# Kernel tuning notes

Hardware: AMD Instinct MI355X
Metric: run time of the kernel (lower is better)

The kernel has to match this reference:

```python
import jax, jax.numpy as jnp
import numpy as np

N_NODES = 50000
N_EDGES = 800000


def setup_inputs() -> dict:
    key = jax.random.key(0)
    ks = jax.random.split(key, 8)
    x = jax.random.normal(ks[0], (N_NODES, 256), dtype=jnp.float32)
    edge_index = jax.random.randint(ks[1], (2, N_EDGES), 0, N_NODES, dtype=jnp.int64)
    edge_weight = jax.random.uniform(ks[2], (N_EDGES,), dtype=jnp.float32)
    # Glorot-style weights for the 3 GCNConv layers: 256->128->64->32
    def glorot(k, fan_in, fan_out):
        s = jnp.sqrt(6.0 / (fan_in + fan_out))
        return jax.random.uniform(k, (fan_in, fan_out), dtype=jnp.float32, minval=-s, maxval=s)
    return {
        "x": x,
        "edge_index": edge_index,
        "edge_weight": edge_weight,
        "W1": glorot(ks[3], 256, 128), "b1": jnp.zeros((128,), jnp.float32),
        "W2": glorot(ks[4], 128, 64),  "b2": jnp.zeros((64,), jnp.float32),
        "W3": glorot(ks[5], 64, 32),   "b3": jnp.zeros((32,), jnp.float32),
    }


def _gcn_forward(x, row, col, ew, params):
    """Stacked GCNConv+ReLU (PyG semantics: add self loops, symmetric norm)."""
    n = x.shape[0]
    loop = jnp.arange(n, dtype=row.dtype)
    row_f = jnp.concatenate([row, loop])            # [E+N] sources
    col_f = jnp.concatenate([col, loop])            # [E+N] targets
    ew_f = jnp.concatenate([ew, jnp.ones((n,), ew.dtype)])
    deg = jax.ops.segment_sum(ew_f, col_f, num_segments=n)
    dinv = jnp.where(deg > 0, jax.lax.rsqrt(deg), 0.0)
    norm = dinv[row_f] * ew_f * dinv[col_f]         # [E+N]
    for W, b in params:
        h = x @ W                                   # [N, d_out] linear first (PyG order)
        msg = h[row_f] * norm[:, None]              # [E+N, d_out] gather + scale
        agg = jax.ops.segment_sum(msg, col_f, num_segments=n)  # scatter-add
        x = jax.nn.relu(agg + b)                    # fused bias + ReLU
    return x


def reference(x, edge_index, edge_weight, W1, b1, W2, b2, W3, b3):
    row, col = edge_index[0], edge_index[1]
    params = [(W1, b1), (W2, b2), (W3, b3)]
    return _gcn_forward(x, row, col, edge_weight, params)
```

## Files before the change

kernel.cpp:

```cpp
#include <hip/hip_runtime.h>
#include <hip/hip_fp16.h>


#define D0 256
#define D1 128
#define D2 64
#define D3 32

#define FIX_SCALE 16777216.0f
#define FIX_INV   (1.0f / 16777216.0f)

typedef _Float16 half8 __attribute__((ext_vector_type(8)));
typedef float floatx4 __attribute__((ext_vector_type(4)));

template <typename SRC>
__device__ __forceinline__ half8 loadA(const SRC* __restrict__ p) {
    if constexpr (sizeof(SRC) == 4) {
        float4 f0 = *(const float4*)p;
        float4 f1 = *(const float4*)(p + 4);
        half8 v;
        v[0] = (_Float16)f0.x; v[1] = (_Float16)f0.y;
        v[2] = (_Float16)f0.z; v[3] = (_Float16)f0.w;
        v[4] = (_Float16)f1.x; v[5] = (_Float16)f1.y;
        v[6] = (_Float16)f1.z; v[7] = (_Float16)f1.w;
        return v;
    } else {
        return *(const half8*)p;
    }
}

template <int K, int BN, typename SRC>
__device__ __forceinline__ void gemm_work(const SRC* __restrict__ X,
                                          const float* __restrict__ W,
                                          _Float16* __restrict__ H, int N,
                                          int w, int totalWaves) {
    constexpr int NC = K / 32;
    constexpr int CG = BN / 32;
    const int lane = threadIdx.x & 63;
    const int quad = lane >> 4;
    const int m = lane & 15;
    const int cg = w & (CG - 1);
    const int nslab = N >> 4;
    const int stride = totalWaves / CG;
    int slab = w / CG;
    if (slab >= nslab) return;
    const int n0 = cg * 32;

    half8 b0[NC], b1[NC];
#pragma unroll
    for (int c = 0; c < NC; ++c) {
#pragma unroll
        for (int j = 0; j < 8; ++j) {
            int k = c * 32 + quad * 8 + j;
            b0[c][j] = (_Float16)W[(size_t)k * BN + n0 + m];
            b1[c][j] = (_Float16)W[(size_t)k * BN + n0 + 16 + m];
        }
    }

    half8 a[NC];
#pragma unroll
    for (int c = 0; c < NC; ++c)
        a[c] = loadA(&X[(size_t)(slab * 16 + m) * K + c * 32 + quad * 8]);

    while (true) {
        const int next = slab + stride;
        half8 an[NC];
        if (next < nslab) {
#pragma unroll
            for (int c = 0; c < NC; ++c)
                an[c] = loadA(&X[(size_t)(next * 16 + m) * K + c * 32 + quad * 8]);
        }

        floatx4 acc0 = (floatx4){0.f, 0.f, 0.f, 0.f};
        floatx4 acc1 = (floatx4){0.f, 0.f, 0.f, 0.f};
#pragma unroll
        for (int c = 0; c < NC; ++c) {
            acc0 = __builtin_amdgcn_mfma_f32_16x16x32_f16(a[c], b0[c], acc0, 0, 0, 0);
            acc1 = __builtin_amdgcn_mfma_f32_16x16x32_f16(a[c], b1[c], acc1, 0, 0, 0);
        }

        const int r0 = slab * 16 + quad * 4;
#pragma unroll
        for (int r = 0; r < 4; ++r) {
            H[(size_t)(r0 + r) * BN + n0 + m]      = (_Float16)acc0[r];
            H[(size_t)(r0 + r) * BN + n0 + 16 + m] = (_Float16)acc1[r];
        }

        if (next >= nslab) break;
        slab = next;
#pragma unroll
        for (int c = 0; c < NC; ++c) a[c] = an[c];
    }
}

__global__ __launch_bounds__(256) void hist_gemm1_kernel(
        const float* __restrict__ x, const float* __restrict__ W1,
        _Float16* __restrict__ h1, int N,
        const int* __restrict__ ei, const float* __restrict__ ew,
        unsigned long long* __restrict__ pk, int* __restrict__ rank, int E,
        int gB) {
    const int b = blockIdx.x;
    if (b < gB) {
        gemm_work<D0, D1, float>(x, W1, h1, N, b * 4 + (threadIdx.x >> 6), gB * 4);
    } else {
        int e = (b - gB) * 256 + threadIdx.x;
        if (e < E) {
            int c = ei[E + e];
            unsigned int wfix = (unsigned int)(ew[e] * FIX_SCALE + 0.5f);
            unsigned long long old =
                atomicAdd(&pk[c], (1ULL << 32) | (unsigned long long)wfix);
            rank[e] = (int)(old >> 32);
        }
    }
}

template <int K, int BN, typename SRC>
__global__ __launch_bounds__(256) void mfma_gemm(const SRC* __restrict__ X,
                                                 const float* __restrict__ W,
                                                 _Float16* __restrict__ H, int N) {
    gemm_work<K, BN, SRC>(X, W, H, N, blockIdx.x * 4 + (threadIdx.x >> 6), gridDim.x * 4);
}

__global__ __launch_bounds__(256) void scan_reduce(const unsigned long long* __restrict__ pk,
                                                   float* __restrict__ dinv,
                                                   int* __restrict__ cnt,
                                                   int* __restrict__ blockSum, int N) {
    __shared__ int s[256];
    const int t = threadIdx.x;
    const int i = blockIdx.x * 256 + t;
    int v = 0;
    if (i < N) {
        unsigned long long p = pk[i];
        float d = (float)(unsigned int)(p & 0xffffffffULL) * FIX_INV + 1.0f;
        dinv[i] = rsqrtf(d);
        v = (int)(p >> 32);
        cnt[i] = v;
    }
    s[t] = v;
    __syncthreads();
#pragma unroll
    for (int off = 128; off > 0; off >>= 1) {
        if (t < off) s[t] += s[t + off];
        __syncthreads();
    }
    if (t == 0) blockSum[blockIdx.x] = s[0];
}

__global__ __launch_bounds__(256) void scan_apply(const int* __restrict__ cnt,
                                                  const int* __restrict__ blockSum,
                                                  int* __restrict__ row_ptr, int N, int B) {
    __shared__ int bs[256];
    __shared__ int s[256];
    const int t = threadIdx.x;
    bs[t] = (t < B) ? blockSum[t] : 0;
    __syncthreads();
#pragma unroll
    for (int off = 1; off < 256; off <<= 1) {
        int u = (t >= off) ? bs[t - off] : 0;
        __syncthreads();
        bs[t] += u;
        __syncthreads();
    }
    const int myOff = (blockIdx.x > 0) ? bs[blockIdx.x - 1] : 0;
    const int i = blockIdx.x * 256 + t;
    const int v = (i < N) ? cnt[i] : 0;
    s[t] = v;
    __syncthreads();
#pragma unroll
    for (int off = 1; off < 256; off <<= 1) {
        int u = (t >= off) ? s[t - off] : 0;
        __syncthreads();
        s[t] += u;
        __syncthreads();
    }
    if (i < N) row_ptr[i] = s[t] - v + myOff;
    if (blockIdx.x == 0 && t == 0) row_ptr[N] = bs[B - 1];
}

__global__ void fill_kernel(const int* __restrict__ ei, const float* __restrict__ ew,
                            const float* __restrict__ dinv,
                            const int* __restrict__ row_ptr, const int* __restrict__ rank,
                            int2* __restrict__ pairs, int E) {
    int e = blockIdx.x * blockDim.x + threadIdx.x;
    if (e < E) {
        int r = ei[e];
        int c = ei[E + e];
        float w = dinv[r] * ew[e] * dinv[c];
        pairs[row_ptr[c] + rank[e]] = make_int2(r, __float_as_int(w));
    }
}

template <int D, typename OUT>
__global__ __launch_bounds__(256) void agg_kernel(const _Float16* __restrict__ H,
                                                  const int* __restrict__ row_ptr,
                                                  const int2* __restrict__ pairs,
                                                  const float* __restrict__ dinv,
                                                  const float* __restrict__ bias,
                                                  OUT* __restrict__ out, int N) {
    constexpr int TPN = D / 8;
    constexpr int NPB = 256 / TPN;
    const int tid = threadIdx.x;
    const int g = tid / TPN;
    const int lane = tid % TPN;
    const int node = blockIdx.x * NPB + g;
    if (node >= N) return;

    const int beg = row_ptr[node];
    const int end = row_ptr[node + 1];
    float acc[8];
#pragma unroll
    for (int j = 0; j < 8; ++j) acc[j] = 0.0f;

    if (end > beg) {
        const int last = end - 1;
        int2 p0 = pairs[beg];
        int2 p1 = pairs[min(beg + 1, last)];
        int2 p2 = pairs[min(beg + 2, last)];
        half8 u0 = *(const half8*)&H[(size_t)p0.x * D + lane * 8];
        half8 u1 = *(const half8*)&H[(size_t)p1.x * D + lane * 8];
        for (int k = beg; k < end; ++k) {
            int2 p3 = pairs[min(k + 3, last)];
            half8 u2 = *(const half8*)&H[(size_t)p2.x * D + lane * 8];
            float w = __int_as_float(p0.y);
#pragma unroll
            for (int j = 0; j < 8; ++j) acc[j] = fmaf(w, (float)u0[j], acc[j]);
            p0 = p1; p1 = p2; p2 = p3;
            u0 = u1; u1 = u2;
        }
    }
    float di = dinv[node];
    float d2 = di * di;
    {
        half8 u = *(const half8*)&H[(size_t)node * D + lane * 8];
#pragma unroll
        for (int j = 0; j < 8; ++j) acc[j] = fmaf(d2, (float)u[j], acc[j]);
    }
    float b[8];
    *(float4*)&b[0] = *(const float4*)&bias[lane * 8];
    *(float4*)&b[4] = *(const float4*)&bias[lane * 8 + 4];
#pragma unroll
    for (int j = 0; j < 8; ++j) acc[j] = fmaxf(acc[j] + b[j], 0.f);

    if constexpr (sizeof(OUT) == 2) {
        half8 o;
#pragma unroll
        for (int j = 0; j < 8; ++j) o[j] = (_Float16)acc[j];
        *(half8*)&out[(size_t)node * D + lane * 8] = o;
    } else {
        float* dst = (float*)&out[(size_t)node * D + lane * 8];
        *(float4*)&dst[0] = make_float4(acc[0], acc[1], acc[2], acc[3]);
        *(float4*)&dst[4] = make_float4(acc[4], acc[5], acc[6], acc[7]);
    }
}

extern "C" void kernel_launch(void* const* d_in, const int* in_sizes, int n_in,
                              void* d_out, int out_size, void* d_ws, size_t ws_size,
                              hipStream_t stream) {
    const float* x   = (const float*)d_in[0];
    const int* ei    = (const int*)d_in[1];
    const float* ew  = (const float*)d_in[2];
    const float* W1  = (const float*)d_in[3];
    const float* b1  = (const float*)d_in[4];
    const float* W2  = (const float*)d_in[5];
    const float* b2  = (const float*)d_in[6];
    const float* W3  = (const float*)d_in[7];
    const float* b3  = (const float*)d_in[8];
    float* out = (float*)d_out;

    const int N = in_sizes[0] / D0;
    const int E = in_sizes[2];
    (void)n_in; (void)out_size; (void)ws_size;

    char* ws = (char*)d_ws;
    size_t off = 0;
    auto carve = [&](size_t bytes) -> void* {
        void* p = (void*)(ws + off);
        off += (bytes + 255) & ~(size_t)255;
        return p;
    };
    unsigned long long* pk = (unsigned long long*)carve((size_t)N * 8);
    float* dinv    = (float*)carve((size_t)N * 4);
    int*   cnt     = (int*)carve((size_t)N * 4);
    int*   row_ptr = (int*)carve((size_t)(N + 1) * 4);
    int*   rank    = (int*)carve((size_t)E * 4);
    int*   bsum    = (int*)carve(256 * 4);
    int2*  pairs   = (int2*)carve((size_t)E * 8);
    _Float16* bufH = (_Float16*)carve((size_t)N * D1 * 2);
    _Float16* bufO = (_Float16*)carve((size_t)N * D1 * 2);

    _Float16* h1   = bufH;
    _Float16* out1 = bufO;
    _Float16* h2   = bufH;
    _Float16* out2 = bufO;
    _Float16* h3   = bufH;

    const int eb = (E + 255) / 256;
    const int scanB = (N + 255) / 256;
    const int gB = 768;

    hipMemsetAsync(pk, 0, (size_t)N * 8, stream);
    hist_gemm1_kernel<<<gB + eb, 256, 0, stream>>>(
        x, W1, h1, N, ei, ew, pk, rank, E, gB);

    scan_reduce<<<scanB, 256, 0, stream>>>(pk, dinv, cnt, bsum, N);
    scan_apply<<<scanB, 256, 0, stream>>>(cnt, bsum, row_ptr, N, scanB);
    fill_kernel<<<eb, 256, 0, stream>>>(ei, ew, dinv, row_ptr, rank, pairs, E);

    agg_kernel<D1, _Float16><<<(N + 15) / 16, 256, 0, stream>>>(h1, row_ptr, pairs, dinv, b1, out1, N);

    mfma_gemm<D1, D2, _Float16><<<gB, 256, 0, stream>>>(out1, W2, h2, N);
    agg_kernel<D2, _Float16><<<(N + 31) / 32, 256, 0, stream>>>(h2, row_ptr, pairs, dinv, b2, out2, N);

    mfma_gemm<D2, D3, _Float16><<<gB, 256, 0, stream>>>(out2, W3, h3, N);
    agg_kernel<D3, float><<<(N + 63) / 64, 256, 0, stream>>>(h3, row_ptr, pairs, dinv, b3, out, N);
}
```

Before: 261.2 us.

## Fuse aggregation with next-layer MFMA GEMM and replicate degree histogram atomics

Fuses each layer's neighbour aggregation, bias and ReLU with the next layer's linear transform. The aggregated tile is staged in shared memory and multiplied by the weight tile with MFMA, which removes the intermediate activation write and reread and two kernel launches. Separately, the degree/count histogram is split into four replicas selected by edge index, to reduce atomic contention on hot nodes. The per-replica offsets are packed into 8-bit fields, so a replica count above 255 would overflow and corrupt the CSR layout.

```diff
diff --git a/kernel.cpp b/kernel.cpp
--- a/kernel.cpp
+++ b/kernel.cpp
@@ -6,6 +6,8 @@
 #define D1 128
 #define D2 64
 #define D3 32
+
+#define NREP 4
 
 #define FIX_SCALE 16777216.0f
 #define FIX_INV   (1.0f / 16777216.0f)
@@ -106,35 +108,39 @@
         int e = (b - gB) * 256 + threadIdx.x;
         if (e < E) {
             int c = ei[E + e];
+            int rep = e & (NREP - 1);
             unsigned int wfix = (unsigned int)(ew[e] * FIX_SCALE + 0.5f);
             unsigned long long old =
-                atomicAdd(&pk[c], (1ULL << 32) | (unsigned long long)wfix);
+                atomicAdd(&pk[(size_t)rep * N + c],
+                          (1ULL << 32) | (unsigned long long)wfix);
             rank[e] = (int)(old >> 32);
         }
     }
-}
-
-template <int K, int BN, typename SRC>
-__global__ __launch_bounds__(256) void mfma_gemm(const SRC* __restrict__ X,
-                                                 const float* __restrict__ W,
-                                                 _Float16* __restrict__ H, int N) {
-    gemm_work<K, BN, SRC>(X, W, H, N, blockIdx.x * 4 + (threadIdx.x >> 6), gridDim.x * 4);
 }
 
 __global__ __launch_bounds__(256) void scan_reduce(const unsigned long long* __restrict__ pk,
                                                    float* __restrict__ dinv,
                                                    int* __restrict__ cnt,
+                                                   unsigned* __restrict__ repbase,
                                                    int* __restrict__ blockSum, int N) {
     __shared__ int s[256];
     const int t = threadIdx.x;
     const int i = blockIdx.x * 256 + t;
     int v = 0;
     if (i < N) {
-        unsigned long long p = pk[i];
-        float d = (float)(unsigned int)(p & 0xffffffffULL) * FIX_INV + 1.0f;
+        unsigned long long p0 = pk[i];
+        unsigned long long p1 = pk[(size_t)N + i];
+        unsigned long long p2 = pk[(size_t)2 * N + i];
+        unsigned long long p3 = pk[(size_t)3 * N + i];
+        unsigned ws = (unsigned)p0 + (unsigned)p1 + (unsigned)p2 + (unsigned)p3;
+        float d = (float)ws * FIX_INV + 1.0f;
         dinv[i] = rsqrtf(d);
-        v = (int)(p >> 32);
+        int c0 = (int)(p0 >> 32), c1 = (int)(p1 >> 32);
+        int c2 = (int)(p2 >> 32), c3 = (int)(p3 >> 32);
+        v = c0 + c1 + c2 + c3;
         cnt[i] = v;
+        repbase[i] = (unsigned)c0 | ((unsigned)(c0 + c1) << 8) |
+                     ((unsigned)(c0 + c1 + c2) << 16);
     }
     s[t] = v;
     __syncthreads();
@@ -180,13 +186,108 @@
 __global__ void fill_kernel(const int* __restrict__ ei, const float* __restrict__ ew,
                             const float* __restrict__ dinv,
                             const int* __restrict__ row_ptr, const int* __restrict__ rank,
+                            const unsigned* __restrict__ repbase,
                             int2* __restrict__ pairs, int E) {
     int e = blockIdx.x * blockDim.x + threadIdx.x;
     if (e < E) {
         int r = ei[e];
         int c = ei[E + e];
         float w = dinv[r] * ew[e] * dinv[c];
-        pairs[row_ptr[c] + rank[e]] = make_int2(r, __float_as_int(w));
+        int rep = e & (NREP - 1);
+        unsigned rb = repbase[c];
+        int base = rep ? (int)((rb >> ((rep - 1) * 8)) & 0xffu) : 0;
+        pairs[row_ptr[c] + base + rank[e]] = make_int2(r, __float_as_int(w));
+    }
+}
+
+template <int DIN, int DOUT>
+__global__ __launch_bounds__(256) void agg_gemm_kernel(
+        const _Float16* __restrict__ H, const int* __restrict__ row_ptr,
+        const int2* __restrict__ pairs, const float* __restrict__ dinv,
+        const float* __restrict__ bias, const float* __restrict__ W,
+        _Float16* __restrict__ Hout, int N) {
+    constexpr int TPN = DIN / 8;
+    constexpr int NPB = 256 / TPN;
+    constexpr int NC  = DIN / 32;
+    constexpr int S   = NPB / 16;
+    constexpr int T   = DOUT / 16;
+    static_assert(S * T == 4, "one tile per wave");
+    __shared__ _Float16 sA[NPB][DIN + 8];
+
+    const int tid = threadIdx.x;
+    const int g = tid / TPN;
+    const int sl = tid % TPN;
+    const int node0 = blockIdx.x * NPB;
+    const int node = node0 + g;
+    const bool valid = node < N;
+
+    const int w = tid >> 6;
+    const int lane = tid & 63;
+    const int q = lane >> 4;
+    const int m = lane & 15;
+    const int s = w & (S - 1);
+    const int t = w / S;
+    half8 bf[NC];
+#pragma unroll
+    for (int c = 0; c < NC; ++c) {
+#pragma unroll
+        for (int j = 0; j < 8; ++j)
+            bf[c][j] = (_Float16)W[(size_t)(c * 32 + q * 8 + j) * DOUT + t * 16 + m];
+    }
+
+    float acc[8];
+#pragma unroll
+    for (int j = 0; j < 8; ++j) acc[j] = 0.0f;
+
+    int beg = 0, end = 0;
+    if (valid) { beg = row_ptr[node]; end = row_ptr[node + 1]; }
+
+    if (end > beg) {
+        const int last = end - 1;
+        int2 p0 = pairs[beg];
+        int2 p1 = pairs[min(beg + 1, last)];
+        int2 p2 = pairs[min(beg + 2, last)];
+        half8 u0 = *(const half8*)&H[(size_t)p0.x * DIN + sl * 8];
+        half8 u1 = *(const half8*)&H[(size_t)p1.x * DIN + sl * 8];
+        for (int k = beg; k < end; ++k) {
+            int2 p3 = pairs[min(k + 3, last)];
+            half8 u2 = *(const half8*)&H[(size_t)p2.x * DIN + sl * 8];
+            float wv = __int_as_float(p0.y);
+#pragma unroll
+            for (int j = 0; j < 8; ++j) acc[j] = fmaf(wv, (float)u0[j], acc[j]);
+            p0 = p1; p1 = p2; p2 = p3;
+            u0 = u1; u1 = u2;
+        }
+    }
+
+    if (valid) {
+        float di = dinv[node];
+        float d2 = di * di;
+        half8 u = *(const half8*)&H[(size_t)node * DIN + sl * 8];
+#pragma unroll
+        for (int j = 0; j < 8; ++j) acc[j] = fmaf(d2, (float)u[j], acc[j]);
+        float bb[8];
+        *(float4*)&bb[0] = *(const float4*)&bias[sl * 8];
+        *(float4*)&bb[4] = *(const float4*)&bias[sl * 8 + 4];
+        half8 o;
+#pragma unroll
+        for (int j = 0; j < 8; ++j) o[j] = (_Float16)fmaxf(acc[j] + bb[j], 0.f);
+        *(half8*)&sA[g][sl * 8] = o;
+    }
+    __syncthreads();
+
+    half8 a[NC];
+#pragma unroll
+    for (int c = 0; c < NC; ++c)
+        a[c] = *(const half8*)&sA[s * 16 + m][c * 32 + q * 8];
+    floatx4 o4 = (floatx4){0.f, 0.f, 0.f, 0.f};
+#pragma unroll
+    for (int c = 0; c < NC; ++c)
+        o4 = __builtin_amdgcn_mfma_f32_16x16x32_f16(a[c], bf[c], o4, 0, 0, 0);
+#pragma unroll
+    for (int r = 0; r < 4; ++r) {
+        const int nr = node0 + s * 16 + q * 4 + r;
+        if (nr < N) Hout[(size_t)nr * DOUT + t * 16 + m] = (_Float16)o4[r];
     }
 }
 
@@ -278,39 +379,39 @@
         off += (bytes + 255) & ~(size_t)255;
         return p;
     };
-    unsigned long long* pk = (unsigned long long*)carve((size_t)N * 8);
+    unsigned long long* pk = (unsigned long long*)carve((size_t)N * NREP * 8);
     float* dinv    = (float*)carve((size_t)N * 4);
     int*   cnt     = (int*)carve((size_t)N * 4);
     int*   row_ptr = (int*)carve((size_t)(N + 1) * 4);
     int*   rank    = (int*)carve((size_t)E * 4);
     int*   bsum    = (int*)carve(256 * 4);
+    unsigned* repbase = (unsigned*)carve((size_t)N * 4);
     int2*  pairs   = (int2*)carve((size_t)E * 8);
     _Float16* bufH = (_Float16*)carve((size_t)N * D1 * 2);
     _Float16* bufO = (_Float16*)carve((size_t)N * D1 * 2);
 
-    _Float16* h1   = bufH;
-    _Float16* out1 = bufO;
-    _Float16* h2   = bufH;
-    _Float16* out2 = bufO;
-    _Float16* h3   = bufH;
+    _Float16* h1 = bufH;
+    _Float16* h2 = bufO;
+    _Float16* h3 = bufH;
 
     const int eb = (E + 255) / 256;
     const int scanB = (N + 255) / 256;
     const int gB = 768;
 
-    hipMemsetAsync(pk, 0, (size_t)N * 8, stream);
+    hipMemsetAsync(pk, 0, (size_t)N * NREP * 8, stream);
     hist_gemm1_kernel<<<gB + eb, 256, 0, stream>>>(
         x, W1, h1, N, ei, ew, pk, rank, E, gB);
 
-    scan_reduce<<<scanB, 256, 0, stream>>>(pk, dinv, cnt, bsum, N);
+    scan_reduce<<<scanB, 256, 0, stream>>>(pk, dinv, cnt, repbase, bsum, N);
     scan_apply<<<scanB, 256, 0, stream>>>(cnt, bsum, row_ptr, N, scanB);
-    fill_kernel<<<eb, 256, 0, stream>>>(ei, ew, dinv, row_ptr, rank, pairs, E);
-
-    agg_kernel<D1, _Float16><<<(N + 15) / 16, 256, 0, stream>>>(h1, row_ptr, pairs, dinv, b1, out1, N);
-
-    mfma_gemm<D1, D2, _Float16><<<gB, 256, 0, stream>>>(out1, W2, h2, N);
-    agg_kernel<D2, _Float16><<<(N + 31) / 32, 256, 0, stream>>>(h2, row_ptr, pairs, dinv, b2, out2, N);
-
-    mfma_gemm<D2, D3, _Float16><<<gB, 256, 0, stream>>>(out2, W3, h3, N);
-    agg_kernel<D3, float><<<(N + 63) / 64, 256, 0, stream>>>(h3, row_ptr, pairs, dinv, b3, out, N);
-}
+    fill_kernel<<<eb, 256, 0, stream>>>(ei, ew, dinv, row_ptr, rank, repbase, pairs, E);
+
+    agg_gemm_kernel<D1, D2><<<(N + 15) / 16, 256, 0, stream>>>(
+        h1, row_ptr, pairs, dinv, b1, W2, h2, N);
+
+    agg_gemm_kernel<D2, D3><<<(N + 31) / 32, 256, 0, stream>>>(
+        h2, row_ptr, pairs, dinv, b2, W3, h3, N);
+
+    agg_kernel<D3, float><<<(N + 63) / 64, 256, 0, stream>>>(
+        h3, row_ptr, pairs, dinv, b3, out, N);
+}
```

Measured after the change: 259.0 us. No clear change (-0.9%).
